# Kernel optimization log

Measured on AMD Instinct MI355X. Metric: run time of the kernel, lower is better.

The kernel has to match this reference:

```python
import jax, jax.numpy as jnp
import numpy as np

VOCAB = 200000
DIM = 300


def setup_inputs() -> dict:
    key = jax.random.key(0)
    k1, k2 = jax.random.split(key)
    wordid = jax.random.randint(k1, (1,), 0, VOCAB, dtype=jnp.int64 if jax.config.jax_enable_x64 else jnp.int32)
    embedding = jax.random.normal(k2, (VOCAB, DIM), dtype=jnp.float32)
    return {"wordid": wordid, "embedding": embedding, "topk": 10}


def reference(wordid, embedding, topk):
    # Embedding lookup: [1, D]
    wordvec = embedding[wordid]
    # Dot-product similarity vs full vocab: [1, V]
    sim_score = jnp.matmul(wordvec, embedding.T)
    # Original code fully sorts scores descending; only the top entries are
    # consumed, so we use top_k (same math for the returned values/indices).
    # +1 because the original skips index 0 (the word itself) and prints
    # entries 1..topk of the sorted list.
    top_vals, top_ids = jax.lax.top_k(sim_score, topk + 1)
    return top_vals, top_ids
```

## Files before the change

### kernel.cpp

```cpp
#include <hip/hip_runtime.h>
#include <hip/hip_bf16.h>


#define V_ROWS 200000
#define D_DIM 300
#define BLOCKS_A 1024
#define THREADS 256
#define WAVES_PER_BLOCK (THREADS / 64)
#define TOTAL_WAVES (BLOCKS_A * WAVES_PER_BLOCK)
#define MAXK 16
#define NCAND (BLOCKS_A * MAXK)

typedef unsigned long long ull;

__device__ __forceinline__ ull pack_vi(float v, int idx) {
    unsigned int u = __float_as_uint(v);
    u ^= (((unsigned int)((int)u >> 31)) | 0x80000000u);
    return ((ull)u << 32) | (unsigned int)(~(unsigned int)idx);
}
__device__ __forceinline__ float unpack_val(ull p) {
    unsigned int u = (unsigned int)(p >> 32);
    u = (u & 0x80000000u) ? (u ^ 0x80000000u) : ~u;
    return __uint_as_float(u);
}
__device__ __forceinline__ int unpack_idx(ull p) {
    return (int)(~(unsigned int)p);
}

__device__ __forceinline__ ull shflx64(ull v, int off) {
    int lo = __shfl_xor((int)(unsigned int)v, off, 64);
    int hi = __shfl_xor((int)(unsigned int)(v >> 32), off, 64);
    return ((ull)(unsigned int)hi << 32) | (unsigned int)lo;
}
__device__ __forceinline__ ull wave_max64(ull v) {
#pragma unroll
    for (int off = 32; off > 0; off >>= 1) {
        ull o = shflx64(v, off);
        v = (o > v) ? o : v;
    }
    return v;
}

__device__ __forceinline__ void insert16(ull (&h)[MAXK], ull key) {
    if (key <= h[MAXK - 1]) return;
    ull prev = ~0ull;
#pragma unroll
    for (int j = 0; j < MAXK; ++j) {
        ull cur = h[j];
        ull mn = (prev < key) ? prev : key;
        h[j] = (mn > cur) ? mn : cur;
        prev = cur;
    }
}

__global__ __launch_bounds__(THREADS) void sim_phase1(const int* __restrict__ wordid,
                                                      const float* __restrict__ emb,
                                                      ull* __restrict__ cands) {
    const int lane = threadIdx.x & 63;
    const int wv = threadIdx.x >> 6;
    const int gwave = blockIdx.x * WAVES_PER_BLOCK + wv;

    const int wid = wordid[0];
    const float4* wrow = (const float4*)(emb + (size_t)wid * D_DIM);
    float4 wv0 = wrow[lane];
    float4 wv1 = make_float4(0.f, 0.f, 0.f, 0.f);
    if (lane < 11) wv1 = wrow[64 + lane];

    ull h[MAXK];
#pragma unroll
    for (int j = 0; j < MAXK; ++j) h[j] = 0ull;

#pragma unroll 2
    for (int row = gwave; row < V_ROWS; row += TOTAL_WAVES) {
        const float4* r4 = (const float4*)(emb + (size_t)row * D_DIM);
        float4 a = r4[lane];
        float s = a.x * wv0.x + a.y * wv0.y + a.z * wv0.z + a.w * wv0.w;
        if (lane < 11) {
            float4 b = r4[64 + lane];
            s += b.x * wv1.x + b.y * wv1.y + b.z * wv1.z + b.w * wv1.w;
        }
#pragma unroll
        for (int off = 32; off > 0; off >>= 1) s += __shfl_xor(s, off, 64);
        insert16(h, pack_vi(s, row));
    }

    __shared__ ull lds[WAVES_PER_BLOCK * MAXK];
    if (lane == 0) {
#pragma unroll
        for (int j = 0; j < MAXK; ++j) lds[wv * MAXK + j] = h[j];
    }
    __syncthreads();
    if (wv == 0) {
        ull cand = lds[lane];
#pragma unroll
        for (int r = 0; r < MAXK; ++r) {
            ull win = wave_max64(cand);
            if (cand == win) cand = 0ull;
            if (lane == 0) cands[(size_t)blockIdx.x * MAXK + r] = win;
        }
    }
}

__global__ __launch_bounds__(THREADS) void sim_phase2(const ull* __restrict__ cands,
                                                      const int* __restrict__ topk,
                                                      float* __restrict__ out) {
    const int t = threadIdx.x;
    const int lane = t & 63;
    const int wv = t >> 6;
    int K = topk[0] + 1;
    if (K > MAXK) K = MAXK;

    ull h[MAXK];
#pragma unroll
    for (int j = 0; j < MAXK; ++j) h[j] = 0ull;
    for (int j = t; j < NCAND; j += THREADS) insert16(h, cands[j]);

    __shared__ ull lds[WAVES_PER_BLOCK * MAXK];
#pragma unroll
    for (int r = 0; r < MAXK; ++r) {
        ull head = h[0];
        ull win = wave_max64(head);
        if (head == win) {
#pragma unroll
            for (int j = 0; j < MAXK - 1; ++j) h[j] = h[j + 1];
            h[MAXK - 1] = 0ull;
        }
        if (lane == 0) lds[wv * MAXK + r] = win;
    }
    __syncthreads();
    if (wv == 0) {
        ull cand = lds[lane];
#pragma unroll
        for (int r = 0; r < MAXK; ++r) {
            ull win = wave_max64(cand);
            if (cand == win) cand = 0ull;
            if (lane == 0 && r < K) {
                out[r] = unpack_val(win);
                out[K + r] = (float)unpack_idx(win);
            }
        }
    }
}

extern "C" void kernel_launch(void* const* d_in, const int* in_sizes, int n_in,
                              void* d_out, int out_size, void* d_ws, size_t ws_size,
                              hipStream_t stream) {
    const int* wordid = (const int*)d_in[0];
    const float* emb = (const float*)d_in[1];
    const int* topk = (const int*)d_in[2];
    float* out = (float*)d_out;
    ull* cands = (ull*)d_ws;

    sim_phase1<<<BLOCKS_A, THREADS, 0, stream>>>(wordid, emb, cands);
    sim_phase2<<<1, THREADS, 0, stream>>>(cands, topk, out);
}
```

Before: 387.5 us.

## Split each wave into four 16-lane groups scoring rows, double block count

Each wave now handles four embedding rows at once, with 16 lanes per row and five float4 loads per lane. This replaces one row per wave, where 53 of 64 lanes sat idle for the tail load. The reduction shuffle shortens to four steps, and the phase-1 grid doubles to 2048 blocks. Per-group top-16 lists are merged through a larger LDS array using a 4-element sorting network. The trade-off is more candidates for the single-block phase 2 to merge and more registers per thread.

```diff
diff --git a/kernel.cpp b/kernel.cpp
--- a/kernel.cpp
+++ b/kernel.cpp
@@ -4,10 +4,11 @@
 
 #define V_ROWS 200000
 #define D_DIM 300
-#define BLOCKS_A 1024
+#define BLOCKS_A 2048
 #define THREADS 256
 #define WAVES_PER_BLOCK (THREADS / 64)
 #define TOTAL_WAVES (BLOCKS_A * WAVES_PER_BLOCK)
+#define ROW_STRIDE (TOTAL_WAVES * 4)
 #define MAXK 16
 #define NCAND (BLOCKS_A * MAXK)
 
@@ -53,49 +54,69 @@
     }
 }
 
+__device__ __forceinline__ float dot4(float4 a, float4 b) {
+    return a.x * b.x + a.y * b.y + a.z * b.z + a.w * b.w;
+}
+
 __global__ __launch_bounds__(THREADS) void sim_phase1(const int* __restrict__ wordid,
                                                       const float* __restrict__ emb,
                                                       ull* __restrict__ cands) {
     const int lane = threadIdx.x & 63;
     const int wv = threadIdx.x >> 6;
+    const int sub = lane & 15;
+    const int grp = lane >> 4;
     const int gwave = blockIdx.x * WAVES_PER_BLOCK + wv;
 
     const int wid = wordid[0];
     const float4* wrow = (const float4*)(emb + (size_t)wid * D_DIM);
-    float4 wv0 = wrow[lane];
-    float4 wv1 = make_float4(0.f, 0.f, 0.f, 0.f);
-    if (lane < 11) wv1 = wrow[64 + lane];
+    float4 w0 = wrow[sub];
+    float4 w1 = wrow[sub + 16];
+    float4 w2 = wrow[sub + 32];
+    float4 w3 = wrow[sub + 48];
+    float4 w4 = make_float4(0.f, 0.f, 0.f, 0.f);
+    if (sub < 11) w4 = wrow[sub + 64];
 
     ull h[MAXK];
 #pragma unroll
     for (int j = 0; j < MAXK; ++j) h[j] = 0ull;
 
-#pragma unroll 2
-    for (int row = gwave; row < V_ROWS; row += TOTAL_WAVES) {
-        const float4* r4 = (const float4*)(emb + (size_t)row * D_DIM);
-        float4 a = r4[lane];
-        float s = a.x * wv0.x + a.y * wv0.y + a.z * wv0.z + a.w * wv0.w;
-        if (lane < 11) {
-            float4 b = r4[64 + lane];
-            s += b.x * wv1.x + b.y * wv1.y + b.z * wv1.z + b.w * wv1.w;
+    for (int base = gwave * 4; base < V_ROWS; base += ROW_STRIDE) {
+        int row = base + grp;
+        bool valid = row < V_ROWS;
+        int srow = valid ? row : V_ROWS - 1;
+        const float4* r4 = (const float4*)(emb + (size_t)srow * D_DIM);
+        float4 a0 = r4[sub];
+        float4 a1 = r4[sub + 16];
+        float4 a2 = r4[sub + 32];
+        float4 a3 = r4[sub + 48];
+        float s = dot4(a0, w0) + dot4(a1, w1) + dot4(a2, w2) + dot4(a3, w3);
+        if (sub < 11) {
+            float4 a4 = r4[sub + 64];
+            s += dot4(a4, w4);
         }
 #pragma unroll
-        for (int off = 32; off > 0; off >>= 1) s += __shfl_xor(s, off, 64);
-        insert16(h, pack_vi(s, row));
+        for (int off = 8; off > 0; off >>= 1) s += __shfl_xor(s, off, 64);
+        ull key = valid ? pack_vi(s, row) : 0ull;
+        insert16(h, key);
     }
 
-    __shared__ ull lds[WAVES_PER_BLOCK * MAXK];
-    if (lane == 0) {
+    __shared__ ull lds[16 * MAXK];
+    if (sub == 0) {
+        int g = (wv << 2) | grp;
 #pragma unroll
-        for (int j = 0; j < MAXK; ++j) lds[wv * MAXK + j] = h[j];
+        for (int j = 0; j < MAXK; ++j) lds[g * MAXK + j] = h[j];
     }
     __syncthreads();
     if (wv == 0) {
-        ull cand = lds[lane];
+        ull m0 = lds[lane], m1 = lds[lane + 64], m2 = lds[lane + 128], m3 = lds[lane + 192];
+        ull t;
+#define CSWP(a, b) { if (b > a) { t = a; a = b; b = t; } }
+        CSWP(m0, m1); CSWP(m2, m3); CSWP(m0, m2); CSWP(m1, m3); CSWP(m1, m2);
+#undef CSWP
 #pragma unroll
         for (int r = 0; r < MAXK; ++r) {
-            ull win = wave_max64(cand);
-            if (cand == win) cand = 0ull;
+            ull win = wave_max64(m0);
+            if (m0 == win) { m0 = m1; m1 = m2; m2 = m3; m3 = 0ull; }
             if (lane == 0) cands[(size_t)blockIdx.x * MAXK + r] = win;
         }
     }
```

Result: slower. 417.0 us (+7.6%).
